# Kernel optimization log

Hardware: AMD Instinct MI355X
Metric: run time of the kernel (lower is better)

## Reference

```python
import jax, jax.numpy as jnp
import numpy as np

# Production-scale dims (see shape_source)
B, H, W, C = 8, 64, 64, 256
KH, KW = 3, 3
BASES = 16
FILTERS = 256


def setup_inputs() -> dict:
    key = jax.random.key(0)
    k1, k2, k3, k4 = jax.random.split(key, 4)
    x = jax.random.normal(k1, (B, H, W, C), dtype=jnp.float32)
    # P: channel-mixing matrix [C, C] (initialized to identity in build, then assigned)
    P = jax.random.normal(k2, (C, C), dtype=jnp.float32) * 0.05
    # Q: per-channel basis kernels [C, kh, kw, bases]
    Q = jax.random.normal(k3, (C, KH, KW, BASES), dtype=jnp.float32) * 0.1
    # S: basis-combination weights [C, bases, filters]
    S = jax.random.normal(k4, (C, BASES, FILTERS), dtype=jnp.float32) * 0.05
    return {"x": x, "P": P, "Q": Q, "S": S}


def reference(x, P, Q, S):
    # --- Step 1: channel mixing (the vectorized_map over calculate_J) ---
    # J[o] = sum_c x[..., c] * P[o, c]  ->  one GEMM over channels
    mixed = jnp.einsum('bhwc,oc->bhwo', x, P)  # [B,H,W,C]

    C_ = P.shape[0]
    kh, kw, bases = Q.shape[1], Q.shape[2], Q.shape[3]

    # --- Step 2: per-channel conv with `bases` basis kernels (the map_fn loop) ---
    # Expressed as ONE grouped (depthwise-style) conv: group c produces outputs
    # [c*bases : (c+1)*bases], matching kernel flatten order (c, b).
    rhs = jnp.transpose(Q, (1, 2, 0, 3)).reshape(kh, kw, 1, C_ * bases)  # HWIO
    dw = jax.lax.conv_general_dilated(
        mixed, rhs, window_strides=(1, 1), padding='VALID',
        dimension_numbers=('NHWC', 'HWIO', 'NHWC'),
        feature_group_count=C_,
    )  # [B, H-kh+1, W-kw+1, C*bases], channel index k = c*bases + b

    b, h, w, _ = dw.shape
    # tau in the original: [B, h, w, bases, C]
    tau = dw.reshape(b, h, w, C_, bases).transpose(0, 1, 2, 4, 3)

    # --- Step 3: basis-weighted combination (the vectorized_map over calculate_O) ---
    # Original flattens tau row-major over (bases, C) and S[:, :, f] row-major over
    # (C, bases), then does an elementwise dot over the flat axis. Replicate exactly.
    Tflat = tau.reshape(b, h, w, bases * C_)          # flat index k = b_idx*C + c
    Sflat = S.reshape(C_ * bases, S.shape[-1])        # flat index k = c*bases + b_idx
    O = jnp.einsum('bhwk,kf->bhwf', Tflat, Sflat)     # [B, h, w, filters]
    return O
```

## Files before the change

kernel.cpp:

```cpp
#include <hip/hip_runtime.h>
#include <hip/hip_bf16.h>

typedef __attribute__((ext_vector_type(4))) float f32x4;
typedef __attribute__((ext_vector_type(8))) short bf16x8;

#define M_TOT 30752

__device__ __forceinline__ unsigned short f2bf(float f) {
  unsigned int u = __float_as_uint(f);
  u = u + 0x7FFF + ((u >> 16) & 1);
  return (unsigned short)(u >> 16);
}

__device__ __forceinline__ void gload16(const void* g, void* l) {
  __builtin_amdgcn_global_load_lds((const __attribute__((address_space(1))) unsigned int*)g,
                                   (__attribute__((address_space(3))) unsigned int*)l,
                                   16, 0, 0);
}

__global__ __launch_bounds__(256) void fused_k(const float* __restrict__ x,
                                               const float* __restrict__ P,
                                               const float* __restrict__ Q,
                                               const float* __restrict__ S,
                                               unsigned short* __restrict__ xb,
                                               unsigned short* __restrict__ K2t) {
  __shared__ float ldsK[256 * 4];
  const int bid = blockIdx.x;
  const int t = threadIdx.x;

  if (bid >= 576) {
    int i = (bid - 576) * 256 + t;
    const f32x4* xp = (const f32x4*)x;
    f32x4 a = xp[2 * i];
    f32x4 b = xp[2 * i + 1];
    bf16x8 o;
    o[0] = (short)f2bf(a[0]); o[1] = (short)f2bf(a[1]);
    o[2] = (short)f2bf(a[2]); o[3] = (short)f2bf(a[3]);
    o[4] = (short)f2bf(b[0]); o[5] = (short)f2bf(b[1]);
    o[6] = (short)f2bf(b[2]); o[7] = (short)f2bf(b[3]);
    ((bf16x8*)xb)[i] = o;
    return;
  }

  const int kk = bid / 64;
  const int f0 = (bid & 63) * 4;
  {
    float k0 = 0.f, k1 = 0.f, k2 = 0.f, k3 = 0.f;
    const float* qp = Q + t * 144 + kk * 16;
    const float* sp = S + (t >> 4) * 4096 + (t & 15) * 256 + f0;
#pragma unroll
    for (int bi = 0; bi < 16; ++bi) {
      float qv = qp[bi];
      const float* s4 = sp + bi * 65536;
      k0 = fmaf(qv, s4[0], k0); k1 = fmaf(qv, s4[1], k1);
      k2 = fmaf(qv, s4[2], k2); k3 = fmaf(qv, s4[3], k3);
    }
    ldsK[t * 4 + 0] = k0; ldsK[t * 4 + 1] = k1;
    ldsK[t * 4 + 2] = k2; ldsK[t * 4 + 3] = k3;
  }
  __syncthreads();
  {
    const int ci = t;
    float acc[4] = {0.f, 0.f, 0.f, 0.f};
#pragma unroll 8
    for (int o = 0; o < 256; ++o) {
      float pv = P[o * 256 + ci];
      acc[0] = fmaf(pv, ldsK[o * 4 + 0], acc[0]);
      acc[1] = fmaf(pv, ldsK[o * 4 + 1], acc[1]);
      acc[2] = fmaf(pv, ldsK[o * 4 + 2], acc[2]);
      acc[3] = fmaf(pv, ldsK[o * 4 + 3], acc[3]);
    }
#pragma unroll
    for (int j = 0; j < 4; ++j)
      K2t[kk * 65536 + (f0 + j) * 256 + ci] = f2bf(acc[j]);
  }
}

__global__ __launch_bounds__(256, 2) void conv_gemm(const unsigned short* __restrict__ xb,
                                                    const unsigned short* __restrict__ K2t,
                                                    float* __restrict__ out) {
  __shared__ __attribute__((aligned(16))) char smem[65536];

  const int tid = threadIdx.x;
  const int lane = tid & 63;
  const int wid = tid >> 6;
  const int sk = wid >> 1;
  const int wn = wid & 1;

  const int wgid = (blockIdx.x & 7) * 61 + (blockIdx.x >> 3);
  if (wgid >= 482) return;
  const int mt = wgid >> 1;
  const int nt = wgid & 1;
  const int m0 = mt * 128;
  const int n0 = nt * 128;

  const int rl = lane & 15;
  const int kg = lane >> 4;

  const int s_src = ((tid & 3) ^ ((tid >> 3) & 3)) * 8;
  int gA0, gA1;
  {
    int m = m0 + (tid >> 2); if (m >= M_TOT) m = M_TOT - 1;
    int b = m / 3844; int rem = m - b * 3844;
    int h = rem / 62; int w = rem - h * 62;
    gA0 = ((b * 64 + h) * 64 + w) * 256 + s_src;
    m = m0 + (tid >> 2) + 64; if (m >= M_TOT) m = M_TOT - 1;
    b = m / 3844; rem = m - b * 3844;
    h = rem / 62; w = rem - h * 62;
    gA1 = ((b * 64 + h) * 64 + w) * 256 + s_src;
  }
  const int fB0 = (n0 + (tid >> 2)) * 256 + s_src;
  const int fB1 = (n0 + (tid >> 2) + 64) * 256 + s_src;

  f32x4 zero = {0.f, 0.f, 0.f, 0.f};
  f32x4 acc[8][4];
#pragma unroll
  for (int i = 0; i < 8; ++i)
#pragma unroll
    for (int j = 0; j < 4; ++j) acc[i][j] = zero;

  const int slotr = (kg ^ ((rl >> 1) & 3)) * 16;
  const int aoff = sk * 8192 + rl * 64 + slotr;
  const int boff = 16384 + sk * 8192 + (wn * 64 + rl) * 64 + slotr;

#define STAGE(t, base)                                                         \
  {                                                                            \
    int kk_ = (t) >> 2, cb_ = (t) & 3;                                         \
    int kh_ = kk_ / 3, kw_ = kk_ - kh_ * 3;                                    \
    int offA_ = kh_ * 16384 + kw_ * 256 + cb_ * 64;                            \
    int offB_ = kk_ * 65536 + cb_ * 64;                                        \
    unsigned short* bA = (unsigned short*)(base);                              \
    unsigned short* bB = (unsigned short*)((char*)(base) + 16384);             \
    gload16(xb + gA0 + offA_,      bA + tid * 8);                              \
    gload16(xb + gA1 + offA_,      bA + (tid + 256) * 8);                      \
    gload16(xb + gA0 + offA_ + 32, bA + (tid + 512) * 8);                      \
    gload16(xb + gA1 + offA_ + 32, bA + (tid + 768) * 8);                      \
    gload16(K2t + offB_ + fB0,      bB + tid * 8);                             \
    gload16(K2t + offB_ + fB1,      bB + (tid + 256) * 8);                     \
    gload16(K2t + offB_ + fB0 + 32, bB + (tid + 512) * 8);                     \
    gload16(K2t + offB_ + fB1 + 32, bB + (tid + 768) * 8);                     \
  }

  STAGE(0, smem);
  asm volatile("s_waitcnt vmcnt(0)" ::: "memory");
  __builtin_amdgcn_sched_barrier(0);
  __builtin_amdgcn_s_barrier();
  __builtin_amdgcn_sched_barrier(0);

  for (int t = 0; t < 36; ++t) {
    char* cur = smem + (t & 1) * 32768;

    if (t < 35) STAGE(t + 1, smem + ((t + 1) & 1) * 32768);
    __builtin_amdgcn_sched_barrier(0);

    bf16x8 bfr[4];
#pragma unroll
    for (int ni = 0; ni < 4; ++ni)
      bfr[ni] = *(const bf16x8*)(cur + boff + ni * 1024);
    bf16x8 a0 = *(const bf16x8*)(cur + aoff);
    bf16x8 a1 = *(const bf16x8*)(cur + aoff + 1024);
#pragma unroll
    for (int j = 0; j < 4; ++j) {
      bf16x8 a2, a3;
      if (j < 3) {
        a2 = *(const bf16x8*)(cur + aoff + (2 * j + 2) * 1024);
        a3 = *(const bf16x8*)(cur + aoff + (2 * j + 3) * 1024);
      }
      __builtin_amdgcn_s_setprio(1);
#pragma unroll
      for (int ni = 0; ni < 4; ++ni)
        acc[2 * j][ni] = __builtin_amdgcn_mfma_f32_16x16x32_bf16(
            a0, bfr[ni], acc[2 * j][ni], 0, 0, 0);
#pragma unroll
      for (int ni = 0; ni < 4; ++ni)
        acc[2 * j + 1][ni] = __builtin_amdgcn_mfma_f32_16x16x32_bf16(
            a1, bfr[ni], acc[2 * j + 1][ni], 0, 0, 0);
      __builtin_amdgcn_s_setprio(0);
      a0 = a2; a1 = a3;
    }

    if (t < 35) {
      __builtin_amdgcn_sched_barrier(0);
      asm volatile("s_waitcnt vmcnt(0)" ::: "memory");
      __builtin_amdgcn_sched_barrier(0);
      __builtin_amdgcn_s_barrier();
      __builtin_amdgcn_sched_barrier(0);
    }
  }

  __syncthreads();

  float* red = (float*)smem;
  if (sk == 1) {
#pragma unroll
    for (int mi = 0; mi < 8; ++mi)
#pragma unroll
      for (int ni = 0; ni < 4; ++ni)
        *(f32x4*)((char*)red + (((wn * 8 + mi) * 4 + ni) * 64 + lane) * 16) =
            acc[mi][ni];
  }
  __syncthreads();
  if (sk == 0) {
#pragma unroll
    for (int mi = 0; mi < 8; ++mi) {
      int mb = m0 + mi * 16 + kg * 4;
#pragma unroll
      for (int ni = 0; ni < 4; ++ni) {
        f32x4 o = *(f32x4*)((char*)red + (((wn * 8 + mi) * 4 + ni) * 64 + lane) * 16);
        o += acc[mi][ni];
        int f = n0 + wn * 64 + ni * 16 + rl;
#pragma unroll
        for (int r = 0; r < 4; ++r) {
          int m = mb + r;
          if (m < M_TOT) out[m * 256 + f] = o[r];
        }
      }
    }
  }
#undef STAGE
}

extern "C" void kernel_launch(void* const* d_in, const int* in_sizes, int n_in,
                              void* d_out, int out_size, void* d_ws, size_t ws_size,
                              hipStream_t stream) {
  const float* x = (const float*)d_in[0];
  const float* P = (const float*)d_in[1];
  const float* Q = (const float*)d_in[2];
  const float* S = (const float*)d_in[3];
  float* out = (float*)d_out;

  char* ws = (char*)d_ws;
  unsigned short* xb  = (unsigned short*)ws;
  unsigned short* K2t = (unsigned short*)(ws + 16777216);

  fused_k<<<4672, 256, 0, stream>>>(x, P, Q, S, xb, K2t);
  conv_gemm<<<488, 256, 0, stream>>>(xb, K2t, out);
}
```

Baseline: 80.02 us.

## Stage input window once per channel block and reuse it across all nine taps

The conv GEMM now tiles M as two full output rows of one image (124 positions) and loads a 4x64-pixel input window into LDS once per 64-channel block. All nine kernel taps read shifted rows from that window instead of reloading an A tile for every tap. Only the weight (B) tile is double-buffered per tap. This aims to cut global/L2 traffic for the activation operand about ninefold. In exchange it wastes 4 of 128 M rows per tile, adds swizzled address math and extra barriers when the window is restaged, and changes the grid to 496 blocks.

```diff
diff --git a/kernel.cpp b/kernel.cpp
--- a/kernel.cpp
+++ b/kernel.cpp
@@ -87,30 +87,44 @@
   const int sk = wid >> 1;
   const int wn = wid & 1;
 
-  const int wgid = (blockIdx.x & 7) * 61 + (blockIdx.x >> 3);
-  if (wgid >= 482) return;
+  const int wgid = (blockIdx.x & 7) * 62 + (blockIdx.x >> 3);
   const int mt = wgid >> 1;
   const int nt = wgid & 1;
-  const int m0 = mt * 128;
+  const int bimg = mt / 31;
+  const int rr2 = mt - bimg * 31;
+  const int m_base = bimg * 3844 + rr2 * 124;
+  const int xrow0 = bimg * 64 + rr2 * 2;
   const int n0 = nt * 128;
 
   const int rl = lane & 15;
   const int kg = lane >> 4;
 
-  const int s_src = ((tid & 3) ^ ((tid >> 3) & 3)) * 8;
-  int gA0, gA1;
+  int wA[8];
   {
-    int m = m0 + (tid >> 2); if (m >= M_TOT) m = M_TOT - 1;
-    int b = m / 3844; int rem = m - b * 3844;
-    int h = rem / 62; int w = rem - h * 62;
-    gA0 = ((b * 64 + h) * 64 + w) * 256 + s_src;
-    m = m0 + (tid >> 2) + 64; if (m >= M_TOT) m = M_TOT - 1;
-    b = m / 3844; rem = m - b * 3844;
-    h = rem / 62; w = rem - h * 62;
-    gA1 = ((b * 64 + h) * 64 + w) * 256 + s_src;
-  }
-  const int fB0 = (n0 + (tid >> 2)) * 256 + s_src;
-  const int fB1 = (n0 + (tid >> 2) + 64) * 256 + s_src;
+    int d8 = ((tid & 7) ^ ((tid >> 3) & 7)) * 8;
+#pragma unroll
+    for (int j = 0; j < 8; ++j) {
+      int row = xrow0 + (j >> 1);
+      int w = (tid >> 3) + 32 * (j & 1);
+      wA[j] = (row * 64 + w) * 256 + d8;
+    }
+  }
+
+  const int s_srcB = ((tid & 3) ^ ((tid >> 3) & 3)) * 8;
+  const int fB0 = (n0 + (tid >> 2)) * 256 + s_srcB;
+  const int fB1 = (n0 + (tid >> 2) + 64) * 256 + s_srcB;
+
+  int s8[8];
+#pragma unroll
+  for (int mi = 0; mi < 8; ++mi) {
+    int lr = mi * 16 + rl; if (lr > 123) lr = 123;
+    int ho = (lr >= 62) ? 1 : 0;
+    s8[mi] = ho * 64 + (lr - ho * 62);
+  }
+  const int csl = sk * 4 + kg;
+
+  const int slotrB = (kg ^ ((rl >> 1) & 3)) * 16;
+  const int boffR = sk * 8192 + (wn * 64 + rl) * 64 + slotrB;
 
   f32x4 zero = {0.f, 0.f, 0.f, 0.f};
   f32x4 acc[8][4];
@@ -119,72 +133,109 @@
 #pragma unroll
     for (int j = 0; j < 4; ++j) acc[i][j] = zero;
 
-  const int slotr = (kg ^ ((rl >> 1) & 3)) * 16;
-  const int aoff = sk * 8192 + rl * 64 + slotr;
-  const int boff = 16384 + sk * 8192 + (wn * 64 + rl) * 64 + slotr;
-
-#define STAGE(t, base)                                                         \
+#define WSTAGE(cb)                                                             \
   {                                                                            \
-    int kk_ = (t) >> 2, cb_ = (t) & 3;                                         \
-    int kh_ = kk_ / 3, kw_ = kk_ - kh_ * 3;                                    \
-    int offA_ = kh_ * 16384 + kw_ * 256 + cb_ * 64;                            \
-    int offB_ = kk_ * 65536 + cb_ * 64;                                        \
-    unsigned short* bA = (unsigned short*)(base);                              \
-    unsigned short* bB = (unsigned short*)((char*)(base) + 16384);             \
-    gload16(xb + gA0 + offA_,      bA + tid * 8);                              \
-    gload16(xb + gA1 + offA_,      bA + (tid + 256) * 8);                      \
-    gload16(xb + gA0 + offA_ + 32, bA + (tid + 512) * 8);                      \
-    gload16(xb + gA1 + offA_ + 32, bA + (tid + 768) * 8);                      \
-    gload16(K2t + offB_ + fB0,      bB + tid * 8);                             \
-    gload16(K2t + offB_ + fB1,      bB + (tid + 256) * 8);                     \
-    gload16(K2t + offB_ + fB0 + 32, bB + (tid + 512) * 8);                     \
-    gload16(K2t + offB_ + fB1 + 32, bB + (tid + 768) * 8);                     \
-  }
-
-  STAGE(0, smem);
+    _Pragma("unroll")                                                          \
+    for (int j = 0; j < 8; ++j)                                                \
+      gload16(xb + wA[j] + (cb) * 64, smem + j * 4096 + tid * 16);             \
+  }
+
+#define STAGE_B(kk2, cb2, base)                                                \
+  {                                                                            \
+    int offB = (kk2) * 65536 + (cb2) * 64;                                     \
+    unsigned short* bB = (unsigned short*)(base);                              \
+    gload16(K2t + offB + fB0,      bB + tid * 8);                              \
+    gload16(K2t + offB + fB1,      bB + (tid + 256) * 8);                      \
+    gload16(K2t + offB + fB0 + 32, bB + (tid + 512) * 8);                      \
+    gload16(K2t + offB + fB1 + 32, bB + (tid + 768) * 8);                      \
+  }
+
+#define AF_READ(dst, mi, koff)                                                 \
+  {                                                                            \
+    int st = s8[mi] + (koff);                                                  \
+    dst = *(const bf16x8*)(smem + st * 128 + ((csl ^ (st & 7)) << 4));         \
+  }
+
+  WSTAGE(0);
+  STAGE_B(0, 0, smem + 32768);
   asm volatile("s_waitcnt vmcnt(0)" ::: "memory");
   __builtin_amdgcn_sched_barrier(0);
   __builtin_amdgcn_s_barrier();
   __builtin_amdgcn_sched_barrier(0);
 
-  for (int t = 0; t < 36; ++t) {
-    char* cur = smem + (t & 1) * 32768;
-
-    if (t < 35) STAGE(t + 1, smem + ((t + 1) & 1) * 32768);
-    __builtin_amdgcn_sched_barrier(0);
-
-    bf16x8 bfr[4];
-#pragma unroll
-    for (int ni = 0; ni < 4; ++ni)
-      bfr[ni] = *(const bf16x8*)(cur + boff + ni * 1024);
-    bf16x8 a0 = *(const bf16x8*)(cur + aoff);
-    bf16x8 a1 = *(const bf16x8*)(cur + aoff + 1024);
-#pragma unroll
-    for (int j = 0; j < 4; ++j) {
-      bf16x8 a2, a3;
-      if (j < 3) {
-        a2 = *(const bf16x8*)(cur + aoff + (2 * j + 2) * 1024);
-        a3 = *(const bf16x8*)(cur + aoff + (2 * j + 3) * 1024);
-      }
-      __builtin_amdgcn_s_setprio(1);
+  int par = 0;
+  for (int cb = 0; cb < 4; ++cb) {
+    for (int kk = 0; kk < 9; ++kk) {
+      const int last = (cb == 3) && (kk == 8);
+      char* curB = smem + 32768 + par * 16384;
+      char* nxtB = smem + 32768 + (par ^ 1) * 16384;
+      const int koff = (kk / 3) * 64 + (kk - (kk / 3) * 3);
+
+      if (!last) {
+        if (kk < 8) {
+          STAGE_B(kk + 1, cb, nxtB);
+        } else {
+          STAGE_B(0, cb + 1, nxtB);
+        }
+      }
+      __builtin_amdgcn_sched_barrier(0);
+
+      bf16x8 bfr[4];
 #pragma unroll
       for (int ni = 0; ni < 4; ++ni)
-        acc[2 * j][ni] = __builtin_amdgcn_mfma_f32_16x16x32_bf16(
-            a0, bfr[ni], acc[2 * j][ni], 0, 0, 0);
-#pragma unroll
-      for (int ni = 0; ni < 4; ++ni)
-        acc[2 * j + 1][ni] = __builtin_amdgcn_mfma_f32_16x16x32_bf16(
-            a1, bfr[ni], acc[2 * j + 1][ni], 0, 0, 0);
-      __builtin_amdgcn_s_setprio(0);
-      a0 = a2; a1 = a3;
-    }
-
-    if (t < 35) {
-      __builtin_amdgcn_sched_barrier(0);
-      asm volatile("s_waitcnt vmcnt(0)" ::: "memory");
-      __builtin_amdgcn_sched_barrier(0);
-      __builtin_amdgcn_s_barrier();
-      __builtin_amdgcn_sched_barrier(0);
+        bfr[ni] = *(const bf16x8*)(curB + boffR + ni * 1024);
+
+      if (kk == 8 && cb < 3) {
+        bf16x8 af[8];
+#pragma unroll
+        for (int mi = 0; mi < 8; ++mi) AF_READ(af[mi], mi, koff);
+        asm volatile("s_waitcnt lgkmcnt(0)" ::: "memory");
+        __builtin_amdgcn_sched_barrier(0);
+        __builtin_amdgcn_s_barrier();
+        __builtin_amdgcn_sched_barrier(0);
+        WSTAGE(cb + 1);
+        __builtin_amdgcn_sched_barrier(0);
+        __builtin_amdgcn_s_setprio(1);
+#pragma unroll
+        for (int mi = 0; mi < 8; ++mi)
+#pragma unroll
+          for (int ni = 0; ni < 4; ++ni)
+            acc[mi][ni] = __builtin_amdgcn_mfma_f32_16x16x32_bf16(
+                af[mi], bfr[ni], acc[mi][ni], 0, 0, 0);
+        __builtin_amdgcn_s_setprio(0);
+      } else {
+        bf16x8 a0, a1;
+        AF_READ(a0, 0, koff);
+        AF_READ(a1, 1, koff);
+#pragma unroll
+        for (int j = 0; j < 4; ++j) {
+          bf16x8 a2, a3;
+          if (j < 3) {
+            AF_READ(a2, 2 * j + 2, koff);
+            AF_READ(a3, 2 * j + 3, koff);
+          }
+          __builtin_amdgcn_s_setprio(1);
+#pragma unroll
+          for (int ni = 0; ni < 4; ++ni)
+            acc[2 * j][ni] = __builtin_amdgcn_mfma_f32_16x16x32_bf16(
+                a0, bfr[ni], acc[2 * j][ni], 0, 0, 0);
+#pragma unroll
+          for (int ni = 0; ni < 4; ++ni)
+            acc[2 * j + 1][ni] = __builtin_amdgcn_mfma_f32_16x16x32_bf16(
+                a1, bfr[ni], acc[2 * j + 1][ni], 0, 0, 0);
+          __builtin_amdgcn_s_setprio(0);
+          a0 = a2; a1 = a3;
+        }
+      }
+
+      if (!last) {
+        __builtin_amdgcn_sched_barrier(0);
+        asm volatile("s_waitcnt vmcnt(0)" ::: "memory");
+        __builtin_amdgcn_sched_barrier(0);
+        __builtin_amdgcn_s_barrier();
+        __builtin_amdgcn_sched_barrier(0);
+      }
+      par ^= 1;
     }
   }
 
@@ -203,7 +254,6 @@
   if (sk == 0) {
 #pragma unroll
     for (int mi = 0; mi < 8; ++mi) {
-      int mb = m0 + mi * 16 + kg * 4;
 #pragma unroll
       for (int ni = 0; ni < 4; ++ni) {
         f32x4 o = *(f32x4*)((char*)red + (((wn * 8 + mi) * 4 + ni) * 64 + lane) * 16);
@@ -211,13 +261,15 @@
         int f = n0 + wn * 64 + ni * 16 + rl;
 #pragma unroll
         for (int r = 0; r < 4; ++r) {
-          int m = mb + r;
-          if (m < M_TOT) out[m * 256 + f] = o[r];
+          int lrow = mi * 16 + kg * 4 + r;
+          if (lrow < 124) out[(m_base + lrow) * 256 + f] = o[r];
         }
       }
     }
   }
-#undef STAGE
+#undef WSTAGE
+#undef STAGE_B
+#undef AF_READ
 }
 
 extern "C" void kernel_launch(void* const* d_in, const int* in_sizes, int n_in,
@@ -234,5 +286,5 @@
   unsigned short* K2t = (unsigned short*)(ws + 16777216);
 
   fused_k<<<4672, 256, 0, stream>>>(x, P, Q, S, xb, K2t);
-  conv_gemm<<<488, 256, 0, stream>>>(xb, K2t, out);
-}
+  conv_gemm<<<496, 256, 0, stream>>>(xb, K2t, out);
+}
```

After: 76.85 us. -4.0%, faster.

## Split conv GEMM tile across 8 waves with 2x2 M/N warp layout

Applied to the files above, without the earlier changes.

Doubles the conv_gemm workgroup to 512 threads, giving 8 waves arranged as 2 K-splits times a 2x2 M/N grid, so each wave computes a 64x64 sub-tile instead of 128x64. This halves per-wave accumulator registers and per-thread global-load count and raises the number of resident waves for latency hiding. In exchange, the A-fragment software prefetch interleaving is removed, more waves contend on barriers and LDS, and the launch bound requests 4 blocks per CU, which 64 KB of LDS per block may not allow.

```diff
diff --git a/kernel.cpp b/kernel.cpp
--- a/kernel.cpp
+++ b/kernel.cpp
@@ -76,7 +76,7 @@
   }
 }
 
-__global__ __launch_bounds__(256, 2) void conv_gemm(const unsigned short* __restrict__ xb,
+__global__ __launch_bounds__(512, 4) void conv_gemm(const unsigned short* __restrict__ xb,
                                                     const unsigned short* __restrict__ K2t,
                                                     float* __restrict__ out) {
   __shared__ __attribute__((aligned(16))) char smem[65536];
@@ -84,7 +84,8 @@
   const int tid = threadIdx.x;
   const int lane = tid & 63;
   const int wid = tid >> 6;
-  const int sk = wid >> 1;
+  const int sk = wid >> 2;
+  const int wm = (wid >> 1) & 1;
   const int wn = wid & 1;
 
   const int wgid = (blockIdx.x & 7) * 61 + (blockIdx.x >> 3);
@@ -98,29 +99,24 @@
   const int kg = lane >> 4;
 
   const int s_src = ((tid & 3) ^ ((tid >> 3) & 3)) * 8;
-  int gA0, gA1;
+  int gA;
   {
     int m = m0 + (tid >> 2); if (m >= M_TOT) m = M_TOT - 1;
     int b = m / 3844; int rem = m - b * 3844;
     int h = rem / 62; int w = rem - h * 62;
-    gA0 = ((b * 64 + h) * 64 + w) * 256 + s_src;
-    m = m0 + (tid >> 2) + 64; if (m >= M_TOT) m = M_TOT - 1;
-    b = m / 3844; rem = m - b * 3844;
-    h = rem / 62; w = rem - h * 62;
-    gA1 = ((b * 64 + h) * 64 + w) * 256 + s_src;
-  }
-  const int fB0 = (n0 + (tid >> 2)) * 256 + s_src;
-  const int fB1 = (n0 + (tid >> 2) + 64) * 256 + s_src;
+    gA = ((b * 64 + h) * 64 + w) * 256 + s_src;
+  }
+  const int fB = (n0 + (tid >> 2)) * 256 + s_src;
 
   f32x4 zero = {0.f, 0.f, 0.f, 0.f};
-  f32x4 acc[8][4];
-#pragma unroll
-  for (int i = 0; i < 8; ++i)
+  f32x4 acc[4][4];
+#pragma unroll
+  for (int i = 0; i < 4; ++i)
 #pragma unroll
     for (int j = 0; j < 4; ++j) acc[i][j] = zero;
 
   const int slotr = (kg ^ ((rl >> 1) & 3)) * 16;
-  const int aoff = sk * 8192 + rl * 64 + slotr;
+  const int aoff = sk * 8192 + (wm * 64 + rl) * 64 + slotr;
   const int boff = 16384 + sk * 8192 + (wn * 64 + rl) * 64 + slotr;
 
 #define STAGE(t, base)                                                         \
@@ -131,14 +127,10 @@
     int offB_ = kk_ * 65536 + cb_ * 64;                                        \
     unsigned short* bA = (unsigned short*)(base);                              \
     unsigned short* bB = (unsigned short*)((char*)(base) + 16384);             \
-    gload16(xb + gA0 + offA_,      bA + tid * 8);                              \
-    gload16(xb + gA1 + offA_,      bA + (tid + 256) * 8);                      \
-    gload16(xb + gA0 + offA_ + 32, bA + (tid + 512) * 8);                      \
-    gload16(xb + gA1 + offA_ + 32, bA + (tid + 768) * 8);                      \
-    gload16(K2t + offB_ + fB0,      bB + tid * 8);                             \
-    gload16(K2t + offB_ + fB1,      bB + (tid + 256) * 8);                     \
-    gload16(K2t + offB_ + fB0 + 32, bB + (tid + 512) * 8);                     \
-    gload16(K2t + offB_ + fB1 + 32, bB + (tid + 768) * 8);                     \
+    gload16(xb + gA + offA_,       bA + tid * 8);                              \
+    gload16(xb + gA + offA_ + 32,  bA + (tid + 512) * 8);                      \
+    gload16(K2t + offB_ + fB,      bB + tid * 8);                              \
+    gload16(K2t + offB_ + fB + 32, bB + (tid + 512) * 8);                      \
   }
 
   STAGE(0, smem);
@@ -153,31 +145,21 @@
     if (t < 35) STAGE(t + 1, smem + ((t + 1) & 1) * 32768);
     __builtin_amdgcn_sched_barrier(0);
 
-    bf16x8 bfr[4];
+    bf16x8 bfr[4], af[4];
 #pragma unroll
     for (int ni = 0; ni < 4; ++ni)
       bfr[ni] = *(const bf16x8*)(cur + boff + ni * 1024);
-    bf16x8 a0 = *(const bf16x8*)(cur + aoff);
-    bf16x8 a1 = *(const bf16x8*)(cur + aoff + 1024);
-#pragma unroll
-    for (int j = 0; j < 4; ++j) {
-      bf16x8 a2, a3;
-      if (j < 3) {
-        a2 = *(const bf16x8*)(cur + aoff + (2 * j + 2) * 1024);
-        a3 = *(const bf16x8*)(cur + aoff + (2 * j + 3) * 1024);
-      }
-      __builtin_amdgcn_s_setprio(1);
+#pragma unroll
+    for (int mi = 0; mi < 4; ++mi)
+      af[mi] = *(const bf16x8*)(cur + aoff + mi * 1024);
+    __builtin_amdgcn_s_setprio(1);
+#pragma unroll
+    for (int mi = 0; mi < 4; ++mi)
 #pragma unroll
       for (int ni = 0; ni < 4; ++ni)
-        acc[2 * j][ni] = __builtin_amdgcn_mfma_f32_16x16x32_bf16(
-            a0, bfr[ni], acc[2 * j][ni], 0, 0, 0);
-#pragma unroll
-      for (int ni = 0; ni < 4; ++ni)
-        acc[2 * j + 1][ni] = __builtin_amdgcn_mfma_f32_16x16x32_bf16(
-            a1, bfr[ni], acc[2 * j + 1][ni], 0, 0, 0);
-      __builtin_amdgcn_s_setprio(0);
-      a0 = a2; a1 = a3;
-    }
+        acc[mi][ni] = __builtin_amdgcn_mfma_f32_16x16x32_bf16(
+            af[mi], bfr[ni], acc[mi][ni], 0, 0, 0);
+    __builtin_amdgcn_s_setprio(0);
 
     if (t < 35) {
       __builtin_amdgcn_sched_barrier(0);
@@ -193,20 +175,20 @@
   float* red = (float*)smem;
   if (sk == 1) {
 #pragma unroll
-    for (int mi = 0; mi < 8; ++mi)
+    for (int mi = 0; mi < 4; ++mi)
 #pragma unroll
       for (int ni = 0; ni < 4; ++ni)
-        *(f32x4*)((char*)red + (((wn * 8 + mi) * 4 + ni) * 64 + lane) * 16) =
+        *(f32x4*)((char*)red + ((((wm * 2 + wn) * 4 + mi) * 4 + ni) * 64 + lane) * 16) =
             acc[mi][ni];
   }
   __syncthreads();
   if (sk == 0) {
 #pragma unroll
-    for (int mi = 0; mi < 8; ++mi) {
-      int mb = m0 + mi * 16 + kg * 4;
+    for (int mi = 0; mi < 4; ++mi) {
+      int mb = m0 + wm * 64 + mi * 16 + kg * 4;
 #pragma unroll
       for (int ni = 0; ni < 4; ++ni) {
-        f32x4 o = *(f32x4*)((char*)red + (((wn * 8 + mi) * 4 + ni) * 64 + lane) * 16);
+        f32x4 o = *(f32x4*)((char*)red + ((((wm * 2 + wn) * 4 + mi) * 4 + ni) * 64 + lane) * 16);
         o += acc[mi][ni];
         int f = n0 + wn * 64 + ni * 16 + rl;
 #pragma unroll
@@ -234,5 +216,5 @@
   unsigned short* K2t = (unsigned short*)(ws + 16777216);
 
   fused_k<<<4672, 256, 0, stream>>>(x, P, Q, S, xb, K2t);
-  conv_gemm<<<488, 256, 0, stream>>>(xb, K2t, out);
-}
+  conv_gemm<<<488, 512, 0, stream>>>(xb, K2t, out);
+}
```

After: 78.05 us. -2.5%, faster.
